# Optimization experiments

Measured on AMD Instinct MI355X. Metric: run time of the kernel, lower is better.

## Reference

```python
import jax, jax.numpy as jnp
import numpy as np

B, S, D, H, G = 2, 4096, 768, 12, 64
HD = D // H
W = 256              # one-sided window (attention_window=512); also the chunk size
NC = S // W
NEG = -1e9
SCALE = 1.0 / np.sqrt(HD)


def setup_inputs() -> dict:
    key = jax.random.key(0)
    ks = jax.random.split(key, 9)
    lin = lambda k: 0.02 * jax.random.normal(k, (D, D), dtype=jnp.float32)
    zb = lambda: jnp.zeros((D,), jnp.float32)
    return {
        "query": jax.random.normal(ks[0], (S, B, D), dtype=jnp.float32),
        # 0 = local token, -1 = global token (wrapper multiplies by -1 -> +1 = global in HF convention)
        "key_padding_mask": jnp.zeros((B, S), jnp.int32).at[:, :G].set(-1),
        "Wq": lin(ks[1]), "bq": zb(),
        "Wk": lin(ks[2]), "bk": zb(),
        "Wv": lin(ks[3]), "bv": zb(),
        "Wqg": lin(ks[4]), "bqg": zb(),
        "Wkg": lin(ks[5]), "bkg": zb(),
        "Wvg": lin(ks[6]), "bvg": zb(),
        "Wo": lin(ks[7]), "bo": zb(),
    }


def _heads(x):  # [B,S,D] -> [B,H,S,HD]
    return x.reshape(B, S, H, HD).transpose(0, 2, 1, 3)


def reference(query, key_padding_mask, Wq, bq, Wk, bk, Wv, bv,
              Wqg, bqg, Wkg, bkg, Wvg, bvg, Wo, bo):
    x = query.transpose(1, 0, 2)                      # [B,S,D]
    attn_mask = -key_padding_mask                     # wrapper: key_padding_mask * -1
    is_pad = attn_mask < 0                            # [B,S]
    is_glb = attn_mask > 0

    q = _heads(x @ Wq + bq) * SCALE                   # [B,H,S,HD]
    k = _heads(x @ Wk + bk)
    v = _heads(x @ Wv + bv)

    # ---- sliding-window scores via overlapping 3-chunk key blocks ----
    qc = q.reshape(B, H, NC, W, HD)
    blk_idx = jnp.arange(NC)[:, None] * W + jnp.arange(3 * W)[None, :]   # [NC,3W] into padded seq
    kpad = jnp.pad(k, ((0, 0), (0, 0), (W, W), (0, 0)))
    vpad = jnp.pad(v, ((0, 0), (0, 0), (W, W), (0, 0)))
    kblk = kpad[:, :, blk_idx]                        # [B,H,NC,3W,HD]
    vblk = vpad[:, :, blk_idx]
    local = jnp.einsum('bhcqd,bhckd->bhcqk', qc, kblk)  # [B,H,NC,W,3W]

    rel = jnp.arange(3 * W)[None, :] - jnp.arange(W)[:, None] - W        # key pos - query pos
    jpos = (jnp.arange(NC)[:, None, None] - 1) * W + jnp.arange(3 * W)[None, None, :]
    band_ok = (jnp.abs(rel)[None] <= W) & (jpos >= 0) & (jpos < S)       # [NC,W,3W]

    key_bad = is_pad | is_glb                         # pad keys masked; global keys handled separately
    kb_blk = jnp.pad(key_bad, ((0, 0), (W, W)), constant_values=True)[:, blk_idx]  # [B,NC,3W]
    ok = band_ok[None, None] & ~kb_blk[:, None, :, None, :]
    local = jnp.where(ok, local, NEG)

    # ---- all queries -> global keys (first G tokens), regular K/V ----
    gsc = jnp.einsum('bhqd,bhgd->bhqg', q, k[:, :, :G])                  # [B,H,S,G]

    scores = jnp.concatenate([gsc, local.reshape(B, H, S, 3 * W)], axis=-1)
    probs = jax.nn.softmax(scores, axis=-1)
    pg = probs[..., :G]
    pl = probs[..., G:].reshape(B, H, NC, W, 3 * W)

    out = jnp.einsum('bhcqk,bhckd->bhcqd', pl, vblk).reshape(B, H, S, HD)
    out = out + jnp.einsum('bhqg,bhgd->bhqd', pg, v[:, :, :G])

    # ---- global query rows: full attention with the dedicated global projections ----
    qg = (_heads(x @ Wqg + bqg) * SCALE)[:, :, :G]    # [B,H,G,HD]
    kg = _heads(x @ Wkg + bkg)
    vg = _heads(x @ Wvg + bvg)
    gq = jnp.einsum('bhgd,bhkd->bhgk', qg, kg)        # [B,H,G,S]
    gq = jnp.where(is_pad[:, None, None, :], NEG, gq)
    gp = jax.nn.softmax(gq, axis=-1)
    out = out.at[:, :, :G].set(jnp.einsum('bhgk,bhkd->bhgd', gp, vg))

    attn_out = out.transpose(0, 2, 1, 3).reshape(B, S, D)   # merge heads -> [B,S,D]
    attn_out = attn_out.transpose(1, 0, 2)                  # back to [S,B,D]
    return attn_out @ Wo + bo                               # wrapper's output Linear
```

## Files before the change

### kernel.cpp

```cpp
#include <hip/hip_runtime.h>
#include <hip/hip_bf16.h>
#include <cstdint>

#define BB 2
#define SS 4096
#define DD 768
#define HH 12
#define GG 64
#define WW 256

typedef __hip_bfloat16 bf16;
typedef unsigned short u16;
typedef __attribute__((ext_vector_type(8))) short short8v;
typedef __attribute__((ext_vector_type(4))) float floatx4;

__device__ __forceinline__ float b2f(u16 u) {
  return __uint_as_float(((unsigned int)u) << 16);
}
__device__ __forceinline__ u16 f2bu(float f) {
  bf16 h = __float2bfloat16(f);
  return *reinterpret_cast<u16*>(&h);
}
__device__ __forceinline__ void async_copy16(const u16* g, u16* l) {
  __builtin_amdgcn_global_load_lds(
      (const __attribute__((address_space(1))) void*)g,
      (__attribute__((address_space(3))) void*)l, 16, 0, 0);
}

struct P7 { const void* p[7]; };

__global__ __launch_bounds__(256) void detect_dtype(const u16* __restrict__ q,
                                                    int* __restrict__ flag) {
  __shared__ int cnt;
  int tid = threadIdx.x;
  if (tid == 0) cnt = 0;
  __syncthreads();
  int bad = 0;
#pragma unroll
  for (int i = 0; i < 16; ++i) {
    float f = b2f(q[tid * 16 + i]);
    if (!isfinite(f) || fabsf(f) > 100.f) bad++;
  }
  atomicAdd(&cnt, bad);
  __syncthreads();
  if (tid == 0) *flag = (cnt > 256) ? 1 : 0;
}

__global__ __launch_bounds__(256) void canon_bf16(const void* __restrict__ src,
                                                  bf16* __restrict__ dst, int n,
                                                  const int* __restrict__ flag) {
  bool f32 = (*flag != 0);
  for (int i = blockIdx.x * 256 + threadIdx.x; i < n; i += gridDim.x * 256) {
    float v = f32 ? ((const float*)src)[i] : b2f(((const u16*)src)[i]);
    dst[i] = __float2bfloat16(v);
  }
}

__global__ __launch_bounds__(256) void transpose_w7(P7 srcs, bf16* __restrict__ dst,
                                                    const int* __restrict__ flag) {
  __shared__ float tile[32][33];
  bool f32 = (*flag != 0);
  const void* src = srcs.p[blockIdx.z];
  bf16* d = dst + (size_t)blockIdx.z * DD * DD;
  int tx = threadIdx.x & 31, ty = threadIdx.x >> 5;
  int k0 = blockIdx.x * 32, n0 = blockIdx.y * 32;
#pragma unroll
  for (int i = 0; i < 32; i += 8) {
    int k = k0 + ty + i, n = n0 + tx;
    float v = f32 ? ((const float*)src)[(size_t)k * DD + n]
                  : b2f(((const u16*)src)[(size_t)k * DD + n]);
    tile[ty + i][tx] = v;
  }
  __syncthreads();
#pragma unroll
  for (int i = 0; i < 32; i += 8) {
    int n = n0 + ty + i, k = k0 + tx;
    d[(size_t)n * DD + k] = __float2bfloat16(tile[tx][ty + i]);
  }
}

__global__ __launch_bounds__(256) void canon_bias7(P7 srcs, bf16* __restrict__ dst,
                                                   const int* __restrict__ flag) {
  bool f32 = (*flag != 0);
  int which = blockIdx.x;
  const void* s = srcs.p[which];
  for (int j = threadIdx.x; j < DD; j += 256)
    dst[which * DD + j] =
        __float2bfloat16(f32 ? ((const float*)s)[j] : b2f(((const u16*)s)[j]));
}

__global__ __launch_bounds__(256) void tr_vt(const bf16* __restrict__ src,
                                             bf16* __restrict__ dst) {
  __shared__ u16 T[64][66];
  int stile = blockIdx.x, bh = blockIdx.y;
  const u16* in = (const u16*)src + (size_t)bh * SS * 64;
  u16* out = (u16*)dst + (size_t)bh * SS * 64;
  int tid = threadIdx.x;
  int srow = tid >> 2, scol = (tid & 3) * 16;
#pragma unroll
  for (int i = 0; i < 4; ++i) {
    ushort4 u = *(const ushort4*)(in + (size_t)(stile * 64 + srow) * 64 + scol + 4 * i);
    *(ushort2*)&T[srow][scol + 4 * i] = make_ushort2(u.x, u.y);
    *(ushort2*)&T[srow][scol + 4 * i + 2] = make_ushort2(u.z, u.w);
  }
  __syncthreads();
  int drow = tid >> 2, dcol = (tid & 3) * 16;
#pragma unroll
  for (int i = 0; i < 4; ++i) {
    ushort4 u;
    u.x = T[dcol + 4 * i + 0][drow];
    u.y = T[dcol + 4 * i + 1][drow];
    u.z = T[dcol + 4 * i + 2][drow];
    u.w = T[dcol + 4 * i + 3][drow];
    *(ushort4*)(out + (size_t)drow * SS + stile * 64 + dcol + 4 * i) = u;
  }
}

__device__ __forceinline__ void gemm_core(const u16* __restrict__ Xp,
                                          const u16* __restrict__ Wp, int bm,
                                          int bn, int tid, u16 (*As)[32],
                                          u16 (*Bs)[32], floatx4 (&acc)[4][4]) {
  int lane = tid & 63, w = tid >> 6, quad = lane >> 4, t = lane & 15;
  int wm = (w >> 1) * 64, wn = (w & 1) * 64;
  int lr = lane >> 2, lc = (lane & 3) * 8;
  for (int k0 = 0; k0 < DD; k0 += 32) {
    __syncthreads();
#pragma unroll
    for (int i = 0; i < 2; ++i) {
      async_copy16(Xp + (size_t)(bm + w * 32 + i * 16 + lr) * DD + k0 + lc,
                   &As[w * 32 + i * 16][0]);
      async_copy16(Wp + (size_t)(bn + w * 32 + i * 16 + lr) * DD + k0 + lc,
                   &Bs[w * 32 + i * 16][0]);
    }
    __syncthreads();
    short8v a[4], bb[4];
#pragma unroll
    for (int mt = 0; mt < 4; ++mt)
      a[mt] = *(const short8v*)&As[wm + mt * 16 + t][quad * 8];
#pragma unroll
    for (int nt = 0; nt < 4; ++nt)
      bb[nt] = *(const short8v*)&Bs[wn + nt * 16 + t][quad * 8];
#pragma unroll
    for (int nt = 0; nt < 4; ++nt)
#pragma unroll
      for (int mt = 0; mt < 4; ++mt)
        acc[nt][mt] = __builtin_amdgcn_mfma_f32_16x16x32_bf16(
            bb[nt], a[mt], acc[nt][mt], 0, 0, 0);
  }
}

__global__ __launch_bounds__(256, 3) void gemm5(const bf16* __restrict__ Xb,
                                                const bf16* __restrict__ Wt0,
                                                const bf16* __restrict__ b0,
                                                bf16* __restrict__ out0) {
  __shared__ __align__(16) u16 As[128][32];
  __shared__ __align__(16) u16 Bs[128][32];
  int tid = threadIdx.x, lane = tid & 63, w = tid >> 6, quad = lane >> 4,
      t = lane & 15;
  int wm = (w >> 1) * 64, wn = (w & 1) * 64;
  int by = blockIdx.y, which = by / 6, bn = (by % 6) * 128,
      bm = blockIdx.x * 128;
  const u16* Wp = (const u16*)Wt0 + (size_t)which * DD * DD;
  const u16* bias = (const u16*)b0 + which * DD;
  bf16* outp = out0 + (size_t)which * BB * HH * SS * 64;
  float scale = (which == 0) ? 0.125f : 1.f;
  floatx4 acc[4][4];
#pragma unroll
  for (int i = 0; i < 4; ++i)
#pragma unroll
    for (int j = 0; j < 4; ++j) acc[i][j] = (floatx4)(0.f);
  gemm_core((const u16*)Xb, Wp, bm, bn, tid, As, Bs, acc);
#pragma unroll
  for (int nt = 0; nt < 4; ++nt) {
    int n0 = bn + wn + nt * 16 + quad * 4;
    int h = n0 >> 6, hd0 = n0 & 63;
    ushort4 bi4 = *(const ushort4*)&bias[n0];
    float bia[4] = {b2f(bi4.x), b2f(bi4.y), b2f(bi4.z), b2f(bi4.w)};
#pragma unroll
    for (int mt = 0; mt < 4; ++mt) {
      int m = bm + wm + mt * 16 + t;
      int s = m >> 1, b = m & 1;
      ushort4 o;
      o.x = f2bu((acc[nt][mt][0] + bia[0]) * scale);
      o.y = f2bu((acc[nt][mt][1] + bia[1]) * scale);
      o.z = f2bu((acc[nt][mt][2] + bia[2]) * scale);
      o.w = f2bu((acc[nt][mt][3] + bia[3]) * scale);
      *(ushort4*)((u16*)outp + (((size_t)(b * HH + h)) * SS + s) * 64 + hd0) = o;
    }
  }
}

template <int MODE>
__global__ __launch_bounds__(256, 3) void gemm_one(const bf16* __restrict__ Xb,
                                                   const bf16* __restrict__ Wtb,
                                                   const bf16* __restrict__ biasb,
                                                   void* __restrict__ outv,
                                                   int Sdim, float scale) {
  __shared__ __align__(16) u16 As[128][32];
  __shared__ __align__(16) u16 Bs[128][32];
  int tid = threadIdx.x, lane = tid & 63, w = tid >> 6, quad = lane >> 4,
      t = lane & 15;
  int wm = (w >> 1) * 64, wn = (w & 1) * 64;
  int bm = blockIdx.x * 128, bn = blockIdx.y * 128;
  floatx4 acc[4][4];
#pragma unroll
  for (int i = 0; i < 4; ++i)
#pragma unroll
    for (int j = 0; j < 4; ++j) acc[i][j] = (floatx4)(0.f);
  gemm_core((const u16*)Xb, (const u16*)Wtb, bm, bn, tid, As, Bs, acc);
  const u16* bias = (const u16*)biasb;
#pragma unroll
  for (int nt = 0; nt < 4; ++nt) {
    int n0 = bn + wn + nt * 16 + quad * 4;
    ushort4 bi4 = *(const ushort4*)&bias[n0];
    float bia[4] = {b2f(bi4.x), b2f(bi4.y), b2f(bi4.z), b2f(bi4.w)};
#pragma unroll
    for (int mt = 0; mt < 4; ++mt) {
      int m = bm + wm + mt * 16 + t;
      if (MODE == 0) {
        int s = m >> 1, b = m & 1;
        int h = n0 >> 6, hd0 = n0 & 63;
        ushort4 o;
        o.x = f2bu((acc[nt][mt][0] + bia[0]) * scale);
        o.y = f2bu((acc[nt][mt][1] + bia[1]) * scale);
        o.z = f2bu((acc[nt][mt][2] + bia[2]) * scale);
        o.w = f2bu((acc[nt][mt][3] + bia[3]) * scale);
        *(ushort4*)((u16*)outv + (((size_t)(b * HH + h)) * Sdim + s) * 64 + hd0) = o;
      } else {
        float4 o;
        o.x = (acc[nt][mt][0] + bia[0]) * scale;
        o.y = (acc[nt][mt][1] + bia[1]) * scale;
        o.z = (acc[nt][mt][2] + bia[2]) * scale;
        o.w = (acc[nt][mt][3] + bia[3]) * scale;
        *(float4*)((float*)outv + (size_t)m * DD + n0) = o;
      }
    }
  }
}

__global__ __launch_bounds__(256, 3) void attn_local128(
    const bf16* __restrict__ qb, const bf16* __restrict__ kb,
    const bf16* __restrict__ vtb, const int* __restrict__ kpm,
    bf16* __restrict__ attnout) {
  __shared__ __align__(16) u16 Qs[128][64];
  __shared__ __align__(16) u16 Ks[64][64];
  __shared__ __align__(16) u16 Vt[64][64];
  __shared__ __align__(16) u16 Ps[128][72];
  __shared__ float Ls[128];
  __shared__ int kbadS[64];
  int bid = blockIdx.x;
  int tile = bid & 31, bh = bid >> 5;
  int b = bh / HH, h = bh % HH;
  int tid = threadIdx.x, lane = tid & 63, w = tid >> 6;
  int quad = lane >> 4, t = lane & 15;
  const u16* qp = (const u16*)qb + (size_t)bh * SS * 64;
  const u16* kp = (const u16*)kb + (size_t)bh * SS * 64;
  const u16* vp = (const u16*)vtb + (size_t)bh * SS * 64;
  int sq0 = GG + tile * 128;
#pragma unroll
  for (int j = 0; j < 4; ++j) {
    int qr = sq0 + w * 32 + j * 8 + (lane >> 3);
    int sr = qr < SS ? qr : SS - 1;
    async_copy16(qp + (size_t)sr * 64 + (lane & 7) * 8, &Qs[w * 32 + j * 8][0]);
  }
  __syncthreads();
  short8v aq[2][2];
#pragma unroll
  for (int st = 0; st < 2; ++st)
#pragma unroll
    for (int ks = 0; ks < 2; ++ks)
      aq[st][ks] = *(const short8v*)&Qs[w * 32 + st * 16 + t][ks * 32 + quad * 8];
  floatx4 O[2][4];
#pragma unroll
  for (int st = 0; st < 2; ++st)
#pragma unroll
    for (int dt = 0; dt < 4; ++dt) O[st][dt] = (floatx4)(0.f);
  float ps[2][4] = {};
  int win_lo = max(sq0 - WW, GG);
  int win_hi = min(sq0 + 127 + WW, SS - 1);
  int kb_lo = win_lo & ~63;
  int iters = ((win_hi - kb_lo) >> 6) + 2;
  for (int it = 0; it < iters; ++it) {
    int kbs = (it == 0) ? 0 : kb_lo + ((it - 1) << 6);
    __syncthreads();
#pragma unroll
    for (int j = 0; j < 2; ++j) {
      async_copy16(kp + (size_t)(kbs + w * 16 + j * 8 + (lane >> 3)) * 64 +
                       (lane & 7) * 8,
                   &Ks[w * 16 + j * 8][0]);
      async_copy16(vp + (size_t)(w * 16 + j * 8 + (lane >> 3)) * SS + kbs +
                       (lane & 7) * 8,
                   &Vt[w * 16 + j * 8][0]);
    }
    if (tid < 64) kbadS[tid] = kpm[b * SS + kbs + tid];
    __syncthreads();
#pragma unroll
    for (int st = 0; st < 2; ++st) {
      floatx4 S[4];
#pragma unroll
      for (int nt = 0; nt < 4; ++nt) {
        S[nt] = (floatx4)(0.f);
#pragma unroll
        for (int ks = 0; ks < 2; ++ks) {
          short8v bk = *(const short8v*)&Ks[nt * 16 + t][ks * 32 + quad * 8];
          S[nt] = __builtin_amdgcn_mfma_f32_16x16x32_bf16(aq[st][ks], bk, S[nt],
                                                          0, 0, 0);
        }
      }
      int prow = w * 32 + st * 16 + quad * 4;
      if (it == 0) {
#pragma unroll
        for (int nt = 0; nt < 4; ++nt)
#pragma unroll
          for (int r = 0; r < 4; ++r) {
            float p = __expf(S[nt][r]);
            ps[st][r] += p;
            Ps[prow + r][((nt ^ quad) << 4) + t] = f2bu(p);
          }
      } else {
#pragma unroll
        for (int r = 0; r < 4; ++r) {
          int qr = sq0 + prow + r;
          int off = kbs + t + WW - qr;
#pragma unroll
          for (int nt = 0; nt < 4; ++nt) {
            int bad = kbadS[nt * 16 + t];
            unsigned u = (unsigned)(off + nt * 16);
            float p = __expf((u <= 2 * WW && bad == 0) ? S[nt][r] : -3.0e38f);
            ps[st][r] += p;
            Ps[prow + r][((nt ^ quad) << 4) + t] = f2bu(p);
          }
        }
      }
    }
    short8v ap[2][2];
#pragma unroll
    for (int st = 0; st < 2; ++st)
#pragma unroll
      for (int ks = 0; ks < 2; ++ks) {
        int chunk = (2 * ks + (quad >> 1)) ^ ((t >> 2) & 3);
        ap[st][ks] = *(const short8v*)&Ps[w * 32 + st * 16 + t]
                                        [(chunk << 4) + ((quad & 1) << 3)];
      }
#pragma unroll
    for (int dt = 0; dt < 4; ++dt) {
#pragma unroll
      for (int ks = 0; ks < 2; ++ks) {
        short8v av = *(const short8v*)&Vt[dt * 16 + t][ks * 32 + quad * 8];
#pragma unroll
        for (int st = 0; st < 2; ++st)
          O[st][dt] = __builtin_amdgcn_mfma_f32_16x16x32_bf16(av, ap[st][ks],
                                                              O[st][dt], 0, 0, 0);
      }
    }
  }
#pragma unroll
  for (int st = 0; st < 2; ++st) {
#pragma unroll
    for (int r = 0; r < 4; ++r)
#pragma unroll
      for (int off = 1; off < 16; off <<= 1) ps[st][r] += __shfl_xor(ps[st][r], off);
    if (t == 0)
#pragma unroll
      for (int r = 0; r < 4; ++r) Ls[w * 32 + st * 16 + quad * 4 + r] = ps[st][r];
  }
#pragma unroll
  for (int st = 0; st < 2; ++st) {
    int q = sq0 + w * 32 + st * 16 + t;
    if (q < SS) {
      float linv = 1.0f / Ls[w * 32 + st * 16 + t];
#pragma unroll
      for (int dt = 0; dt < 4; ++dt) {
        ushort4 o;
        o.x = f2bu(O[st][dt][0] * linv);
        o.y = f2bu(O[st][dt][1] * linv);
        o.z = f2bu(O[st][dt][2] * linv);
        o.w = f2bu(O[st][dt][3] * linv);
        *(ushort4*)((u16*)attnout + ((size_t)q * BB + b) * DD + h * 64 +
                    dt * 16 + quad * 4) = o;
      }
    }
  }
}

__global__ __launch_bounds__(256) void attn_glb(
    const bf16* __restrict__ qgb, const bf16* __restrict__ kgb,
    const bf16* __restrict__ vtb, const int* __restrict__ kpm,
    float* __restrict__ part) {
  __shared__ __align__(16) u16 Qs[64][72];
  __shared__ __align__(16) u16 Ks[64][72];
  __shared__ __align__(16) u16 Vt[64][72];
  __shared__ __align__(16) u16 Ps[64][72];
  __shared__ int kbadS[64];
  int bid = blockIdx.x;
  int bh = bid >> 4, seg = bid & 15;
  int b = bh / HH;
  int tid = threadIdx.x, lane = tid & 63, w = tid >> 6;
  int quad = lane >> 4, t = lane & 15;
  const u16* qp = (const u16*)qgb + (size_t)bh * GG * 64;
  const u16* kp = (const u16*)kgb + (size_t)bh * SS * 64;
  const u16* vp = (const u16*)vtb + (size_t)bh * SS * 64;
  int srow = tid >> 2, scol = (tid & 3) * 16;
#pragma unroll
  for (int i = 0; i < 4; ++i)
    *(ushort4*)&Qs[srow][scol + 4 * i] =
        *(const ushort4*)(qp + (size_t)srow * 64 + scol + 4 * i);
  __syncthreads();
  short8v aq[2];
#pragma unroll
  for (int ks = 0; ks < 2; ++ks)
    aq[ks] = *(const short8v*)&Qs[16 * w + t][ks * 32 + quad * 8];
  floatx4 O[4];
#pragma unroll
  for (int i = 0; i < 4; ++i) O[i] = (floatx4)(0.f);
  float ps[4] = {0.f, 0.f, 0.f, 0.f};
  for (int it = 0; it < 4; ++it) {
    int kbs = (seg << 8) + (it << 6);
    ushort4 ku[4], vu[4];
#pragma unroll
    for (int i = 0; i < 4; ++i) {
      ku[i] = *(const ushort4*)(kp + (size_t)(kbs + srow) * 64 + scol + 4 * i);
      vu[i] = *(const ushort4*)(vp + (size_t)srow * SS + kbs + scol + 4 * i);
    }
    int kbval = (tid < 64) ? kpm[b * SS + kbs + tid] : 0;
    __syncthreads();
#pragma unroll
    for (int i = 0; i < 4; ++i) {
      *(ushort4*)&Ks[srow][scol + 4 * i] = ku[i];
      *(ushort4*)&Vt[srow][scol + 4 * i] = vu[i];
    }
    if (tid < 64) kbadS[tid] = kbval;
    __syncthreads();
    floatx4 S[4];
#pragma unroll
    for (int nt = 0; nt < 4; ++nt) {
      S[nt] = (floatx4)(0.f);
#pragma unroll
      for (int ks = 0; ks < 2; ++ks) {
        short8v bk = *(const short8v*)&Ks[nt * 16 + t][ks * 32 + quad * 8];
        S[nt] = __builtin_amdgcn_mfma_f32_16x16x32_bf16(aq[ks], bk, S[nt], 0, 0, 0);
      }
    }
#pragma unroll
    for (int nt = 0; nt < 4; ++nt) {
      int bad = kbadS[nt * 16 + t];
#pragma unroll
      for (int r = 0; r < 4; ++r) {
        float p = __expf((bad <= 0) ? S[nt][r] : -3.0e38f);
        ps[r] += p;
        Ps[16 * w + quad * 4 + r][((nt ^ quad) << 4) + t] = f2bu(p);
      }
    }
    short8v ap[2];
#pragma unroll
    for (int ks = 0; ks < 2; ++ks) {
      int chunk = (2 * ks + (quad >> 1)) ^ ((t >> 2) & 3);
      ap[ks] = *(const short8v*)&Ps[16 * w + t][(chunk << 4) + ((quad & 1) << 3)];
    }
#pragma unroll
    for (int dt = 0; dt < 4; ++dt)
#pragma unroll
      for (int ks = 0; ks < 2; ++ks) {
        short8v bv = *(const short8v*)&Vt[dt * 16 + t][ks * 32 + quad * 8];
        O[dt] = __builtin_amdgcn_mfma_f32_16x16x32_bf16(ap[ks], bv, O[dt], 0, 0, 0);
      }
  }
#pragma unroll
  for (int r = 0; r < 4; ++r)
#pragma unroll
    for (int off = 1; off < 16; off <<= 1) ps[r] += __shfl_xor(ps[r], off);
  float* pO = part + (size_t)bid * 4160;
#pragma unroll
  for (int dt = 0; dt < 4; ++dt)
#pragma unroll
    for (int r = 0; r < 4; ++r)
      pO[(16 * w + quad * 4 + r) * 64 + dt * 16 + t] = O[dt][r];
  if (t == 0)
#pragma unroll
    for (int r = 0; r < 4; ++r) pO[4096 + 16 * w + quad * 4 + r] = ps[r];
}

__global__ __launch_bounds__(256) void attn_comb(const float* __restrict__ part,
                                                 bf16* __restrict__ attnout) {
  int tid = threadIdx.x, lane = tid & 63, w = tid >> 6;
  int idx = blockIdx.x * 4 + w;
  int bh = idx >> 6, row = idx & 63;
  int b = bh / HH, h = bh % HH;
  float o = 0.f, L = 0.f;
#pragma unroll
  for (int s16 = 0; s16 < 16; ++s16) {
    const float* p = part + (size_t)(bh * 16 + s16) * 4160;
    o += p[(row << 6) + lane];
    L += p[4096 + row];
  }
  attnout[((size_t)row * BB + b) * DD + h * 64 + lane] = __float2bfloat16(o / L);
}

extern "C" void kernel_launch(void* const* d_in, const int* in_sizes, int n_in,
                              void* d_out, int out_size, void* d_ws,
                              size_t ws_size, hipStream_t stream) {
  const int* kpm = (const int*)d_in[1];
  float* outp = (float*)d_out;
  const size_t SZ = (size_t)BB * HH * SS * 64;
  const size_t WSZ = (size_t)DD * DD;
  bf16* p = (bf16*)d_ws;
  bf16* cQ = p; p += SZ;
  bf16* cWt = p; p += 7 * WSZ;
  bf16* cB = p; p += 7 * DD;
  bf16* q = p; p += SZ;
  bf16* k = p; p += SZ;
  bf16* v = p; p += SZ;
  bf16* kg = p; p += SZ;
  bf16* vg = p; p += SZ;
  bf16* qg = p; p += (size_t)BB * HH * GG * 64;
  bf16* attnout = p; p += SZ;
  float* part = (float*)p;
  int* flag = (int*)(part + (size_t)384 * 4160);
  bf16* vT = cQ;
  bf16* vgT = v;
  const float SC = 0.125f;
  dim3 blk(256);

  P7 wsrc{{d_in[2], d_in[4], d_in[6], d_in[10], d_in[12], d_in[8], d_in[14]}};
  P7 bsrc{{d_in[3], d_in[5], d_in[7], d_in[11], d_in[13], d_in[9], d_in[15]}};

  detect_dtype<<<1, blk, 0, stream>>>((const u16*)d_in[0], flag);
  canon_bf16<<<dim3(2048), blk, 0, stream>>>(d_in[0], cQ, (int)SZ, flag);
  transpose_w7<<<dim3(24, 24, 7), blk, 0, stream>>>(wsrc, cWt, flag);
  canon_bias7<<<dim3(7), blk, 0, stream>>>(bsrc, cB, flag);

  gemm5<<<dim3(64, 30), blk, 0, stream>>>(cQ, cWt, cB, q);
  gemm_one<0><<<dim3(1, 6), blk, 0, stream>>>(cQ, cWt + 5 * WSZ, cB + 5 * DD,
                                              qg, GG, SC);
  tr_vt<<<dim3(64, 24), blk, 0, stream>>>(v, vT);
  tr_vt<<<dim3(64, 24), blk, 0, stream>>>(vg, vgT);
  attn_local128<<<dim3(24 * 32), blk, 0, stream>>>(q, k, vT, kpm, attnout);
  attn_glb<<<dim3(BB * HH * 16), blk, 0, stream>>>(qg, kg, vgT, kpm, part);
  attn_comb<<<dim3(BB * HH * 16), blk, 0, stream>>>(part, attnout);
  gemm_one<1><<<dim3(64, 6), blk, 0, stream>>>(attnout, cWt + 6 * WSZ,
                                               cB + 6 * DD, outp, 0, 1.f);
}
```

Measured before the change: 304.4 us.

## Fuse prep kernels and switch GEMMs to 32x32x16 MFMA with swizzled LDS

Merges the input-canonicalisation, weight-transpose and bias kernels into one prep launch. It folds the global-query projection into the batched projection GEMM grid and merges the two V transposes into one launch. The projection and output GEMMs move from 16x16x32 to 32x32x16 MFMA, with a 64-wide K step and XOR-swizzled LDS to cut bank conflicts. The aim is fewer launches, fewer LDS reads and fewer barrier rounds per K. The cost is a larger shared-memory footprint per block and more complex epilogue indexing.

```diff
diff --git a/kernel.cpp b/kernel.cpp
--- a/kernel.cpp
+++ b/kernel.cpp
@@ -13,6 +13,7 @@
 typedef unsigned short u16;
 typedef __attribute__((ext_vector_type(8))) short short8v;
 typedef __attribute__((ext_vector_type(4))) float floatx4;
+typedef __attribute__((ext_vector_type(16))) float floatx16;
 
 __device__ __forceinline__ float b2f(u16 u) {
   return __uint_as_float(((unsigned int)u) << 16);
@@ -46,55 +47,58 @@
   if (tid == 0) *flag = (cnt > 256) ? 1 : 0;
 }
 
-__global__ __launch_bounds__(256) void canon_bf16(const void* __restrict__ src,
-                                                  bf16* __restrict__ dst, int n,
-                                                  const int* __restrict__ flag) {
+__global__ __launch_bounds__(256) void prep(P7 wsrc, P7 bsrc,
+                                            const void* __restrict__ qsrc,
+                                            bf16* __restrict__ cWt,
+                                            bf16* __restrict__ cB,
+                                            bf16* __restrict__ cQ,
+                                            const int* __restrict__ flag) {
   bool f32 = (*flag != 0);
-  for (int i = blockIdx.x * 256 + threadIdx.x; i < n; i += gridDim.x * 256) {
-    float v = f32 ? ((const float*)src)[i] : b2f(((const u16*)src)[i]);
-    dst[i] = __float2bfloat16(v);
-  }
-}
-
-__global__ __launch_bounds__(256) void transpose_w7(P7 srcs, bf16* __restrict__ dst,
-                                                    const int* __restrict__ flag) {
-  __shared__ float tile[32][33];
-  bool f32 = (*flag != 0);
-  const void* src = srcs.p[blockIdx.z];
-  bf16* d = dst + (size_t)blockIdx.z * DD * DD;
-  int tx = threadIdx.x & 31, ty = threadIdx.x >> 5;
-  int k0 = blockIdx.x * 32, n0 = blockIdx.y * 32;
-#pragma unroll
-  for (int i = 0; i < 32; i += 8) {
-    int k = k0 + ty + i, n = n0 + tx;
-    float v = f32 ? ((const float*)src)[(size_t)k * DD + n]
-                  : b2f(((const u16*)src)[(size_t)k * DD + n]);
-    tile[ty + i][tx] = v;
-  }
-  __syncthreads();
-#pragma unroll
-  for (int i = 0; i < 32; i += 8) {
-    int n = n0 + ty + i, k = k0 + tx;
-    d[(size_t)n * DD + k] = __float2bfloat16(tile[tx][ty + i]);
-  }
-}
-
-__global__ __launch_bounds__(256) void canon_bias7(P7 srcs, bf16* __restrict__ dst,
-                                                   const int* __restrict__ flag) {
-  bool f32 = (*flag != 0);
-  int which = blockIdx.x;
-  const void* s = srcs.p[which];
-  for (int j = threadIdx.x; j < DD; j += 256)
-    dst[which * DD + j] =
-        __float2bfloat16(f32 ? ((const float*)s)[j] : b2f(((const u16*)s)[j]));
-}
-
-__global__ __launch_bounds__(256) void tr_vt(const bf16* __restrict__ src,
-                                             bf16* __restrict__ dst) {
+  int z = blockIdx.z;
+  if (z < 7) {
+    __shared__ float tile[32][33];
+    const void* src = wsrc.p[z];
+    bf16* d = cWt + (size_t)z * DD * DD;
+    int tx = threadIdx.x & 31, ty = threadIdx.x >> 5;
+    int k0 = blockIdx.x * 32, n0 = blockIdx.y * 32;
+#pragma unroll
+    for (int i = 0; i < 32; i += 8) {
+      int k = k0 + ty + i, n = n0 + tx;
+      float v = f32 ? ((const float*)src)[(size_t)k * DD + n]
+                    : b2f(((const u16*)src)[(size_t)k * DD + n]);
+      tile[ty + i][tx] = v;
+    }
+    __syncthreads();
+#pragma unroll
+    for (int i = 0; i < 32; i += 8) {
+      int n = n0 + ty + i, k = k0 + tx;
+      d[(size_t)n * DD + k] = __float2bfloat16(tile[tx][ty + i]);
+    }
+  } else if (z == 7) {
+    int bidx = blockIdx.x + 24 * blockIdx.y;
+    const int n = BB * HH * SS * 64;
+    for (int i = bidx * 256 + threadIdx.x; i < n; i += 576 * 256) {
+      float v = f32 ? ((const float*)qsrc)[i] : b2f(((const u16*)qsrc)[i]);
+      cQ[i] = __float2bfloat16(v);
+    }
+  } else {
+    int which = blockIdx.x;
+    if (which >= 7 || blockIdx.y != 0) return;
+    const void* s = bsrc.p[which];
+    for (int j = threadIdx.x; j < DD; j += 256)
+      cB[which * DD + j] =
+          __float2bfloat16(f32 ? ((const float*)s)[j] : b2f(((const u16*)s)[j]));
+  }
+}
+
+__global__ __launch_bounds__(256) void tr_vt2(const bf16* __restrict__ s0,
+                                              bf16* __restrict__ d0,
+                                              const bf16* __restrict__ s1,
+                                              bf16* __restrict__ d1) {
   __shared__ u16 T[64][66];
   int stile = blockIdx.x, bh = blockIdx.y;
-  const u16* in = (const u16*)src + (size_t)bh * SS * 64;
-  u16* out = (u16*)dst + (size_t)bh * SS * 64;
+  const u16* in = (const u16*)(blockIdx.z ? s1 : s0) + (size_t)bh * SS * 64;
+  u16* out = (u16*)(blockIdx.z ? d1 : d0) + (size_t)bh * SS * 64;
   int tid = threadIdx.x;
   int srow = tid >> 2, scol = (tid & 3) * 16;
 #pragma unroll
@@ -104,135 +108,150 @@
     *(ushort2*)&T[srow][scol + 4 * i + 2] = make_ushort2(u.z, u.w);
   }
   __syncthreads();
-  int drow = tid >> 2, dcol = (tid & 3) * 16;
 #pragma unroll
   for (int i = 0; i < 4; ++i) {
     ushort4 u;
-    u.x = T[dcol + 4 * i + 0][drow];
-    u.y = T[dcol + 4 * i + 1][drow];
-    u.z = T[dcol + 4 * i + 2][drow];
-    u.w = T[dcol + 4 * i + 3][drow];
-    *(ushort4*)(out + (size_t)drow * SS + stile * 64 + dcol + 4 * i) = u;
-  }
-}
-
-__device__ __forceinline__ void gemm_core(const u16* __restrict__ Xp,
-                                          const u16* __restrict__ Wp, int bm,
-                                          int bn, int tid, u16 (*As)[32],
-                                          u16 (*Bs)[32], floatx4 (&acc)[4][4]) {
-  int lane = tid & 63, w = tid >> 6, quad = lane >> 4, t = lane & 15;
+    u.x = T[scol + 4 * i + 0][srow];
+    u.y = T[scol + 4 * i + 1][srow];
+    u.z = T[scol + 4 * i + 2][srow];
+    u.w = T[scol + 4 * i + 3][srow];
+    *(ushort4*)(out + (size_t)srow * SS + stile * 64 + scol + 4 * i) = u;
+  }
+}
+
+__device__ __forceinline__ void stage_tile(const u16* __restrict__ gp,
+                                           size_t row0, u16 (*Ls)[64], int w,
+                                           int lane, int k0) {
+#pragma unroll
+  for (int j = 0; j < 4; ++j)
+    async_copy16(gp + (row0 + (size_t)(w * 32 + j * 8 + (lane >> 3))) * DD + k0 +
+                     (((lane & 7) ^ ((lane >> 3) & 7)) << 3),
+                 &Ls[w * 32 + j * 8][0]);
+}
+__device__ __forceinline__ short8v lda(u16 (*Ls)[64], int base, int lane, int kk) {
+  int row = base + (lane & 31);
+  int c = (kk >> 3) + (lane >> 5);
+  return *(const short8v*)&Ls[row][((c ^ (row & 7)) << 3)];
+}
+
+__device__ __forceinline__ void gemm_core2(const u16* __restrict__ Xp,
+                                           const u16* __restrict__ Wp, int bm,
+                                           int bn, int tid, u16 (*As)[64],
+                                           u16 (*Bs)[64], floatx16 (&acc)[2][2]) {
+  int lane = tid & 63, w = tid >> 6;
   int wm = (w >> 1) * 64, wn = (w & 1) * 64;
-  int lr = lane >> 2, lc = (lane & 3) * 8;
-  for (int k0 = 0; k0 < DD; k0 += 32) {
-    __syncthreads();
-#pragma unroll
-    for (int i = 0; i < 2; ++i) {
-      async_copy16(Xp + (size_t)(bm + w * 32 + i * 16 + lr) * DD + k0 + lc,
-                   &As[w * 32 + i * 16][0]);
-      async_copy16(Wp + (size_t)(bn + w * 32 + i * 16 + lr) * DD + k0 + lc,
-                   &Bs[w * 32 + i * 16][0]);
-    }
-    __syncthreads();
-    short8v a[4], bb[4];
-#pragma unroll
-    for (int mt = 0; mt < 4; ++mt)
-      a[mt] = *(const short8v*)&As[wm + mt * 16 + t][quad * 8];
-#pragma unroll
-    for (int nt = 0; nt < 4; ++nt)
-      bb[nt] = *(const short8v*)&Bs[wn + nt * 16 + t][quad * 8];
-#pragma unroll
-    for (int nt = 0; nt < 4; ++nt)
-#pragma unroll
-      for (int mt = 0; mt < 4; ++mt)
-        acc[nt][mt] = __builtin_amdgcn_mfma_f32_16x16x32_bf16(
-            bb[nt], a[mt], acc[nt][mt], 0, 0, 0);
-  }
-}
-
-__global__ __launch_bounds__(256, 3) void gemm5(const bf16* __restrict__ Xb,
+  for (int k0 = 0; k0 < DD; k0 += 64) {
+    __syncthreads();
+    stage_tile(Wp, (size_t)bn, As, w, lane, k0);
+    stage_tile(Xp, (size_t)bm, Bs, w, lane, k0);
+    __syncthreads();
+#pragma unroll
+    for (int kk = 0; kk < 64; kk += 16) {
+      short8v a0 = lda(As, wn, lane, kk);
+      short8v a1 = lda(As, wn + 32, lane, kk);
+      short8v b0 = lda(Bs, wm, lane, kk);
+      short8v b1 = lda(Bs, wm + 32, lane, kk);
+      acc[0][0] = __builtin_amdgcn_mfma_f32_32x32x16_bf16(a0, b0, acc[0][0], 0, 0, 0);
+      acc[0][1] = __builtin_amdgcn_mfma_f32_32x32x16_bf16(a0, b1, acc[0][1], 0, 0, 0);
+      acc[1][0] = __builtin_amdgcn_mfma_f32_32x32x16_bf16(a1, b0, acc[1][0], 0, 0, 0);
+      acc[1][1] = __builtin_amdgcn_mfma_f32_32x32x16_bf16(a1, b1, acc[1][1], 0, 0, 0);
+    }
+  }
+}
+
+__global__ __launch_bounds__(256, 4) void gemm5(const bf16* __restrict__ Xb,
                                                 const bf16* __restrict__ Wt0,
                                                 const bf16* __restrict__ b0,
-                                                bf16* __restrict__ out0) {
-  __shared__ __align__(16) u16 As[128][32];
-  __shared__ __align__(16) u16 Bs[128][32];
-  int tid = threadIdx.x, lane = tid & 63, w = tid >> 6, quad = lane >> 4,
-      t = lane & 15;
+                                                bf16* __restrict__ out0,
+                                                bf16* __restrict__ qg) {
+  __shared__ __align__(16) u16 As[128][64];
+  __shared__ __align__(16) u16 Bs[128][64];
+  int tid = threadIdx.x, lane = tid & 63, w = tid >> 6;
   int wm = (w >> 1) * 64, wn = (w & 1) * 64;
-  int by = blockIdx.y, which = by / 6, bn = (by % 6) * 128,
-      bm = blockIdx.x * 128;
+  int which, bn, bm;
+  if (blockIdx.y == 30) {
+    if (blockIdx.x >= 6) return;
+    which = 5;
+    bn = blockIdx.x * 128;
+    bm = 0;
+  } else {
+    which = blockIdx.y / 6;
+    bn = (blockIdx.y % 6) * 128;
+    bm = blockIdx.x * 128;
+  }
   const u16* Wp = (const u16*)Wt0 + (size_t)which * DD * DD;
   const u16* bias = (const u16*)b0 + which * DD;
-  bf16* outp = out0 + (size_t)which * BB * HH * SS * 64;
-  float scale = (which == 0) ? 0.125f : 1.f;
-  floatx4 acc[4][4];
-#pragma unroll
-  for (int i = 0; i < 4; ++i)
-#pragma unroll
-    for (int j = 0; j < 4; ++j) acc[i][j] = (floatx4)(0.f);
-  gemm_core((const u16*)Xb, Wp, bm, bn, tid, As, Bs, acc);
-#pragma unroll
-  for (int nt = 0; nt < 4; ++nt) {
-    int n0 = bn + wn + nt * 16 + quad * 4;
-    int h = n0 >> 6, hd0 = n0 & 63;
-    ushort4 bi4 = *(const ushort4*)&bias[n0];
-    float bia[4] = {b2f(bi4.x), b2f(bi4.y), b2f(bi4.z), b2f(bi4.w)};
-#pragma unroll
-    for (int mt = 0; mt < 4; ++mt) {
-      int m = bm + wm + mt * 16 + t;
+  int Sdim = (which == 5) ? GG : SS;
+  u16* outp = (which == 5) ? (u16*)qg
+                           : (u16*)out0 + (size_t)which * BB * HH * SS * 64;
+  float scale = (which == 0 || which == 5) ? 0.125f : 1.f;
+  floatx16 acc[2][2];
+#pragma unroll
+  for (int i = 0; i < 2; ++i)
+#pragma unroll
+    for (int j = 0; j < 2; ++j) acc[i][j] = (floatx16)(0.f);
+  gemm_core2((const u16*)Xb, Wp, bm, bn, tid, As, Bs, acc);
+#pragma unroll
+  for (int nt = 0; nt < 2; ++nt) {
+    int n0 = bn + wn + nt * 32;
+    int h = n0 >> 6;
+    int nsub = (n0 & 63) + ((lane >> 5) << 2);
+    ushort4 bi[4];
+#pragma unroll
+    for (int g = 0; g < 4; ++g)
+      bi[g] = *(const ushort4*)&bias[n0 + ((lane >> 5) << 2) + g * 8];
+#pragma unroll
+    for (int mt = 0; mt < 2; ++mt) {
+      int m = bm + wm + mt * 32 + (lane & 31);
       int s = m >> 1, b = m & 1;
-      ushort4 o;
-      o.x = f2bu((acc[nt][mt][0] + bia[0]) * scale);
-      o.y = f2bu((acc[nt][mt][1] + bia[1]) * scale);
-      o.z = f2bu((acc[nt][mt][2] + bia[2]) * scale);
-      o.w = f2bu((acc[nt][mt][3] + bia[3]) * scale);
-      *(ushort4*)((u16*)outp + (((size_t)(b * HH + h)) * SS + s) * 64 + hd0) = o;
-    }
-  }
-}
-
-template <int MODE>
-__global__ __launch_bounds__(256, 3) void gemm_one(const bf16* __restrict__ Xb,
+      u16* outb = outp + ((size_t)(b * HH + h) * Sdim + s) * 64 + nsub;
+#pragma unroll
+      for (int g = 0; g < 4; ++g) {
+        ushort4 o;
+        o.x = f2bu((acc[nt][mt][4 * g + 0] + b2f(bi[g].x)) * scale);
+        o.y = f2bu((acc[nt][mt][4 * g + 1] + b2f(bi[g].y)) * scale);
+        o.z = f2bu((acc[nt][mt][4 * g + 2] + b2f(bi[g].z)) * scale);
+        o.w = f2bu((acc[nt][mt][4 * g + 3] + b2f(bi[g].w)) * scale);
+        *(ushort4*)(outb + g * 8) = o;
+      }
+    }
+  }
+}
+
+__global__ __launch_bounds__(256, 4) void gemm_out(const bf16* __restrict__ Xb,
                                                    const bf16* __restrict__ Wtb,
                                                    const bf16* __restrict__ biasb,
-                                                   void* __restrict__ outv,
-                                                   int Sdim, float scale) {
-  __shared__ __align__(16) u16 As[128][32];
-  __shared__ __align__(16) u16 Bs[128][32];
-  int tid = threadIdx.x, lane = tid & 63, w = tid >> 6, quad = lane >> 4,
-      t = lane & 15;
+                                                   float* __restrict__ outv) {
+  __shared__ __align__(16) u16 As[128][64];
+  __shared__ __align__(16) u16 Bs[128][64];
+  int tid = threadIdx.x, lane = tid & 63, w = tid >> 6;
   int wm = (w >> 1) * 64, wn = (w & 1) * 64;
   int bm = blockIdx.x * 128, bn = blockIdx.y * 128;
-  floatx4 acc[4][4];
-#pragma unroll
-  for (int i = 0; i < 4; ++i)
-#pragma unroll
-    for (int j = 0; j < 4; ++j) acc[i][j] = (floatx4)(0.f);
-  gemm_core((const u16*)Xb, (const u16*)Wtb, bm, bn, tid, As, Bs, acc);
+  floatx16 acc[2][2];
+#pragma unroll
+  for (int i = 0; i < 2; ++i)
+#pragma unroll
+    for (int j = 0; j < 2; ++j) acc[i][j] = (floatx16)(0.f);
+  gemm_core2((const u16*)Xb, (const u16*)Wtb, bm, bn, tid, As, Bs, acc);
   const u16* bias = (const u16*)biasb;
 #pragma unroll
-  for (int nt = 0; nt < 4; ++nt) {
-    int n0 = bn + wn + nt * 16 + quad * 4;
-    ushort4 bi4 = *(const ushort4*)&bias[n0];
-    float bia[4] = {b2f(bi4.x), b2f(bi4.y), b2f(bi4.z), b2f(bi4.w)};
-#pragma unroll
-    for (int mt = 0; mt < 4; ++mt) {
-      int m = bm + wm + mt * 16 + t;
-      if (MODE == 0) {
-        int s = m >> 1, b = m & 1;
-        int h = n0 >> 6, hd0 = n0 & 63;
-        ushort4 o;
-        o.x = f2bu((acc[nt][mt][0] + bia[0]) * scale);
-        o.y = f2bu((acc[nt][mt][1] + bia[1]) * scale);
-        o.z = f2bu((acc[nt][mt][2] + bia[2]) * scale);
-        o.w = f2bu((acc[nt][mt][3] + bia[3]) * scale);
-        *(ushort4*)((u16*)outv + (((size_t)(b * HH + h)) * Sdim + s) * 64 + hd0) = o;
-      } else {
+  for (int nt = 0; nt < 2; ++nt) {
+    int n0 = bn + wn + nt * 32 + ((lane >> 5) << 2);
+    ushort4 bi[4];
+#pragma unroll
+    for (int g = 0; g < 4; ++g) bi[g] = *(const ushort4*)&bias[n0 + g * 8];
+#pragma unroll
+    for (int mt = 0; mt < 2; ++mt) {
+      int m = bm + wm + mt * 32 + (lane & 31);
+      float* outb = outv + (size_t)m * DD + n0;
+#pragma unroll
+      for (int g = 0; g < 4; ++g) {
         float4 o;
-        o.x = (acc[nt][mt][0] + bia[0]) * scale;
-        o.y = (acc[nt][mt][1] + bia[1]) * scale;
-        o.z = (acc[nt][mt][2] + bia[2]) * scale;
-        o.w = (acc[nt][mt][3] + bia[3]) * scale;
-        *(float4*)((float*)outv + (size_t)m * DD + n0) = o;
+        o.x = acc[nt][mt][4 * g + 0] + b2f(bi[g].x);
+        o.y = acc[nt][mt][4 * g + 1] + b2f(bi[g].y);
+        o.z = acc[nt][mt][4 * g + 2] + b2f(bi[g].z);
+        o.w = acc[nt][mt][4 * g + 3] + b2f(bi[g].w);
+        *(float4*)(outb + g * 8) = o;
       }
     }
   }
@@ -518,25 +537,18 @@
   int* flag = (int*)(part + (size_t)384 * 4160);
   bf16* vT = cQ;
   bf16* vgT = v;
-  const float SC = 0.125f;
   dim3 blk(256);
+  (void)kg; (void)vg;
 
   P7 wsrc{{d_in[2], d_in[4], d_in[6], d_in[10], d_in[12], d_in[8], d_in[14]}};
   P7 bsrc{{d_in[3], d_in[5], d_in[7], d_in[11], d_in[13], d_in[9], d_in[15]}};
 
   detect_dtype<<<1, blk, 0, stream>>>((const u16*)d_in[0], flag);
-  canon_bf16<<<dim3(2048), blk, 0, stream>>>(d_in[0], cQ, (int)SZ, flag);
-  transpose_w7<<<dim3(24, 24, 7), blk, 0, stream>>>(wsrc, cWt, flag);
-  canon_bias7<<<dim3(7), blk, 0, stream>>>(bsrc, cB, flag);
-
-  gemm5<<<dim3(64, 30), blk, 0, stream>>>(cQ, cWt, cB, q);
-  gemm_one<0><<<dim3(1, 6), blk, 0, stream>>>(cQ, cWt + 5 * WSZ, cB + 5 * DD,
-                                              qg, GG, SC);
-  tr_vt<<<dim3(64, 24), blk, 0, stream>>>(v, vT);
-  tr_vt<<<dim3(64, 24), blk, 0, stream>>>(vg, vgT);
+  prep<<<dim3(24, 24, 9), blk, 0, stream>>>(wsrc, bsrc, d_in[0], cWt, cB, cQ, flag);
+  gemm5<<<dim3(64, 31), blk, 0, stream>>>(cQ, cWt, cB, q, qg);
+  tr_vt2<<<dim3(64, 24, 2), blk, 0, stream>>>(v, vT, vg, vgT);
   attn_local128<<<dim3(24 * 32), blk, 0, stream>>>(q, k, vT, kpm, attnout);
   attn_glb<<<dim3(BB * HH * 16), blk, 0, stream>>>(qg, kg, vgT, kpm, part);
   attn_comb<<<dim3(BB * HH * 16), blk, 0, stream>>>(part, attnout);
-  gemm_one<1><<<dim3(64, 6), blk, 0, stream>>>(attnout, cWt + 6 * WSZ,
-                                               cB + 6 * DD, outp, 0, 1.f);
-}
+  gemm_out<<<dim3(64, 6), blk, 0, stream>>>(attnout, cWt + 6 * WSZ, cB + 6 * DD, outp);
+}
```

After: 300.7 us. About the same (-1.2%).
